# Kernel optimization log

Hardware: AMD Instinct MI355X
Metric: run time of the kernel (lower is better)

The kernel has to match this reference:

```python
import jax, jax.numpy as jnp
import numpy as np

N = 100000      # nodes
E = 1600000     # edges
F_IN = 64       # num_features
H = 64          # hidden_channels
NG = 64         # graphs in batch
ALPHA = 0.5


def _lin_init(key, fan_in, fan_out):
    kw, kb = jax.random.split(key)
    bound = 1.0 / np.sqrt(fan_in)
    w = jax.random.uniform(kw, (fan_in, fan_out), jnp.float32, -bound, bound)
    b = jax.random.uniform(kb, (fan_out,), jnp.float32, -bound, bound)
    return w, b


def setup_inputs() -> dict:
    key = jax.random.key(0)
    ks = jax.random.split(key, 12)
    x = jax.random.normal(ks[0], (N, F_IN), dtype=jnp.float32)
    edge_index = jax.random.randint(ks[1], (2, E), 0, N, dtype=jnp.int32)
    batch = jnp.sort(jax.random.randint(ks[2], (N,), 0, NG, dtype=jnp.int32))
    w1s, b1s = _lin_init(ks[3], F_IN, H)
    w1d, b1d = _lin_init(ks[4], F_IN, H)
    w2s, b2s = _lin_init(ks[5], H, H)
    w2d, b2d = _lin_init(ks[6], H, H)
    w3s, b3s = _lin_init(ks[7], H, H)
    w3d, b3d = _lin_init(ks[8], H, H)
    wl1, bl1 = _lin_init(ks[9], H, 5)
    wl2, bl2 = _lin_init(ks[10], 5, 1)
    return dict(x=x, edge_index=edge_index, batch=batch,
                w1s=w1s, b1s=b1s, w1d=w1d, b1d=b1d,
                w2s=w2s, b2s=b2s, w2d=w2d, b2d=b2d,
                w3s=w3s, b3s=b3s, w3d=w3d, b3d=b3d,
                wl1=wl1, bl1=bl1, wl2=wl2, bl2=bl2)


def _dir_gcn_conv(x, row, col, ws, bs, wd, bd):
    # directional norm: D_out^{-1/2} A D_in^{-1/2} (and same recipe for A^T)
    ones = jnp.ones((row.shape[0],), x.dtype)
    deg_out = jax.ops.segment_sum(ones, row, num_segments=N)  # row-sums of A
    deg_in = jax.ops.segment_sum(ones, col, num_segments=N)   # col-sums of A
    r_out = jnp.where(deg_out > 0, deg_out ** -0.5, 0.0)
    r_in = jnp.where(deg_in > 0, deg_in ** -0.5, 0.0)
    norm = r_out[row] * r_in[col]  # per-edge weight; identical for A and A^T norms
    msg = norm[:, None] * x[col]                       # [E, F]
    adj_x = jax.ops.segment_sum(msg, row, num_segments=N)
    msg_t = norm[:, None] * x[row]
    adj_t_x = jax.ops.segment_sum(msg_t, col, num_segments=N)
    return ALPHA * (adj_x @ ws + bs) + (1.0 - ALPHA) * (adj_t_x @ wd + bd)


def reference(x, edge_index, batch,
              w1s, b1s, w1d, b1d,
              w2s, b2s, w2d, b2d,
              w3s, b3s, w3d, b3d,
              wl1, bl1, wl2, bl2):
    row, col = edge_index[0], edge_index[1]
    h = jax.nn.relu(_dir_gcn_conv(x, row, col, w1s, b1s, w1d, b1d))
    h = jax.nn.relu(_dir_gcn_conv(h, row, col, w2s, b2s, w2d, b2d))
    h = jax.nn.relu(_dir_gcn_conv(h, row, col, w3s, b3s, w3d, b3d))
    g = jax.ops.segment_max(h, batch, num_segments=NG)  # global max pool [NG, H]
    g = jax.nn.relu(g @ wl1 + bl1)
    return g @ wl2 + bl2  # [NG, 1]
```

## Files before the change

### kernel.cpp

```cpp
#include <hip/hip_runtime.h>

#define N_NODES 100000
#define N_EDGES 1600000
#define EPAD    (N_EDGES + NB * BW)
#define HDIM    64
#define NGRAPH  64
#define BW      256
#define NB      391
#define NBLK    256
#define CHUNK   ((N_EDGES + NBLK - 1) / NBLK)
#define MTILES  (N_NODES / 16)

typedef _Float16 h16;
typedef _Float16 h16x4 __attribute__((ext_vector_type(4)));
typedef _Float16 h16x8 __attribute__((ext_vector_type(8)));
typedef float    f32x4 __attribute__((ext_vector_type(4)));

__global__ __launch_bounds__(512) void bucket_count(const int* __restrict__ ei,
                                                    int* __restrict__ cntTabA,
                                                    int* __restrict__ cntTabT) {
    __shared__ int cA[NB], cT[NB];
    const int tid = threadIdx.x;
    for (int i = tid; i < NB; i += 512) { cA[i] = 0; cT[i] = 0; }
    __syncthreads();
    const int e0 = blockIdx.x * CHUNK, e1 = min(e0 + CHUNK, N_EDGES);
    for (int e = e0 + tid; e < e1; e += 512) {
        int r = ei[e];
        int c = ei[N_EDGES + e];
        atomicAdd(&cA[r >> 8], 1);
        atomicAdd(&cT[c >> 8], 1);
    }
    __syncthreads();
    for (int b = tid; b < NB; b += 512) {
        cntTabA[b * NBLK + blockIdx.x] = cA[b];
        cntTabT[b * NBLK + blockIdx.x] = cT[b];
    }
}

__global__ __launch_bounds__(256) void chunk_scan(int* __restrict__ cntTabA,
                                                  int* __restrict__ cntTabT,
                                                  int* __restrict__ tot) {
    __shared__ int s[256];
    const int b = blockIdx.x, d = blockIdx.y, tid = threadIdx.x;
    int* tab = d ? cntTabT : cntTabA;
    int v = tab[b * NBLK + tid];
    s[tid] = v;
    __syncthreads();
    for (int off = 1; off < 256; off <<= 1) {
        int t = (tid >= off) ? s[tid - off] : 0;
        __syncthreads();
        s[tid] += t;
        __syncthreads();
    }
    tab[b * NBLK + tid] = s[tid] - v;
    if (tid == 255) tot[d * 512 + b] = s[255];
}

__global__ __launch_bounds__(512) void start_scan(const int* __restrict__ tot,
                                                  int* __restrict__ bktStartA,
                                                  int* __restrict__ bktStartT) {
    __shared__ int s[512];
    const int tid = threadIdx.x;
    int v = (tid < NB) ? tot[tid] : 0;
    s[tid] = v;
    __syncthreads();
    for (int off = 1; off < 512; off <<= 1) {
        int t = (tid >= off) ? s[tid - off] : 0;
        __syncthreads();
        s[tid] += t;
        __syncthreads();
    }
    if (tid < NB) bktStartA[tid] = s[tid] - v;
    if (tid == 0) bktStartA[NB] = N_EDGES;
    __syncthreads();
    int v2 = (tid < NB) ? tot[512 + tid] : 0;
    s[tid] = v2;
    __syncthreads();
    for (int off = 1; off < 512; off <<= 1) {
        int t = (tid >= off) ? s[tid - off] : 0;
        __syncthreads();
        s[tid] += t;
        __syncthreads();
    }
    if (tid < NB) bktStartT[tid] = s[tid] - v2;
    if (tid == 0) bktStartT[NB] = N_EDGES;
}

__global__ __launch_bounds__(512) void bucketize_write(const int* __restrict__ ei,
                                                       const int* __restrict__ cntTabA,
                                                       const int* __restrict__ cntTabT,
                                                       const int* __restrict__ bktStartA,
                                                       const int* __restrict__ bktStartT,
                                                       int2* __restrict__ bktA,
                                                       int2* __restrict__ bktT) {
    __shared__ int bA[NB], bT[NB];
    const int tid = threadIdx.x;
    for (int i = tid; i < NB; i += 512) {
        bA[i] = bktStartA[i] + cntTabA[i * NBLK + blockIdx.x];
        bT[i] = bktStartT[i] + cntTabT[i * NBLK + blockIdx.x];
    }
    __syncthreads();
    const int e0 = blockIdx.x * CHUNK, e1 = min(e0 + CHUNK, N_EDGES);
    for (int e = e0 + tid; e < e1; e += 512) {
        int r = ei[e];
        int c = ei[N_EDGES + e];
        int pA = atomicAdd(&bA[r >> 8], 1);
        bktA[pA] = make_int2(r, c);
        int pT = atomicAdd(&bT[c >> 8], 1);
        bktT[pT] = make_int2(c, r);
    }
}

__global__ __launch_bounds__(256) void bucket_deg_ptr(
        const int* __restrict__ bktStartA, const int* __restrict__ bktStartT,
        const int2* __restrict__ bktA, const int2* __restrict__ bktT,
        int* __restrict__ deg_out, int* __restrict__ deg_in,
        float* __restrict__ r_out, float* __restrict__ r_in,
        int* __restrict__ rowptrP, int* __restrict__ colptrP) {
    __shared__ int c[BW];
    __shared__ int s[256];
    const int b = blockIdx.x, d = blockIdx.y, tid = threadIdx.x;
    const int* bs = d ? bktStartT : bktStartA;
    const int2* bkt = d ? bktT : bktA;
    int* deg = d ? deg_in : deg_out;
    float* rr = d ? r_in : r_out;
    int* ptr = d ? colptrP : rowptrP;
    const int node0 = b * BW;
    c[tid] = 0;
    __syncthreads();
    const int i0 = bs[b], i1 = bs[b + 1];
    for (int i = i0 + tid; i < i1; i += 256) atomicAdd(&c[bkt[i].x - node0], 1);
    __syncthreads();
    int n = node0 + tid, dg = c[tid];
    int pad = dg + (dg & 1);
    if (n < N_NODES) {
        deg[n] = dg;
        rr[n] = dg > 0 ? rsqrtf((float)dg) : 0.0f;
    } else pad = 0;
    s[tid] = pad;
    __syncthreads();
    for (int off = 1; off < 256; off <<= 1) {
        int t = (tid >= off) ? s[tid - off] : 0;
        __syncthreads();
        s[tid] += t;
        __syncthreads();
    }
    if (n < N_NODES) ptr[n] = i0 + b * BW + (s[tid] - pad);
}

__global__ __launch_bounds__(512) void bucket_scatter(
        const int* __restrict__ rowptrP, const int* __restrict__ colptrP,
        const float* __restrict__ r_out, const float* __restrict__ r_in,
        const int* __restrict__ bktStartA, const int* __restrict__ bktStartT,
        const int2* __restrict__ bktA, const int2* __restrict__ bktT,
        int2* __restrict__ recA, int2* __restrict__ recT) {
    __shared__ int cur[BW];
    __shared__ float rwt[BW];
    const int b = blockIdx.x, d = blockIdx.y, tid = threadIdx.x;
    const int* ptr = d ? colptrP : rowptrP;
    const float* rt = d ? r_in : r_out;
    const float* rs = d ? r_out : r_in;
    const int* bs = d ? bktStartT : bktStartA;
    const int2* bkt = d ? bktT : bktA;
    int2* rec = d ? recT : recA;
    const int node0 = b * BW;
    if (tid < BW) {
        int n = node0 + tid;
        cur[tid] = (n < N_NODES) ? ptr[n] : 0;
        rwt[tid] = (n < N_NODES) ? rt[n] : 0.0f;
    }
    __syncthreads();
    const int i0 = bs[b], i1 = bs[b + 1];
    for (int i = i0 + tid; i < i1; i += 512) {
        int2 e = bkt[i];
        float w = rwt[e.x - node0] * rs[e.y];
        int p = atomicAdd(&cur[e.x - node0], 1);
        rec[p] = make_int2(e.y << 7, __float_as_int(w));
    }
}

__global__ __launch_bounds__(256) void cast_kernel(const float4* __restrict__ x,
                                                   h16x4* __restrict__ xh,
                                                   unsigned* __restrict__ g) {
    if (blockIdx.x == 0) {
        for (int j = threadIdx.x; j < NGRAPH * HDIM; j += 256) g[j] = 0u;
    }
    int i = blockIdx.x * 256 + threadIdx.x;
    if (i < N_NODES * 16) {
        float4 v = x[i];
        h16x4 o;
        o.x = (h16)v.x; o.y = (h16)v.y; o.z = (h16)v.z; o.w = (h16)v.w;
        xh[i] = o;
    }
}

__global__ __launch_bounds__(256) void wprep_kernel(
        const float* __restrict__ w1s, const float* __restrict__ w1d,
        const float* __restrict__ w2s, const float* __restrict__ w2d,
        const float* __restrict__ w3s, const float* __restrict__ w3d,
        const float* __restrict__ b1s, const float* __restrict__ b1d,
        const float* __restrict__ b2s, const float* __restrict__ b2d,
        const float* __restrict__ b3s, const float* __restrict__ b3d,
        h16* __restrict__ WT, float* __restrict__ bc) {
    const int l = blockIdx.y;
    const float* ws = l == 0 ? w1s : l == 1 ? w2s : w3s;
    const float* wd = l == 0 ? w1d : l == 1 ? w2d : w3d;
    int e = blockIdx.x * 256 + threadIdx.x;
    if (e < 8192) {
        int f = e >> 7, k = e & 127;
        float v = (k < 64) ? ws[k * 64 + f] : wd[(k - 64) * 64 + f];
        WT[l * 8192 + f * 128 + k] = (h16)(0.5f * v);
    }
    if (blockIdx.x == 0 && threadIdx.x < 64) {
        const float* bs = l == 0 ? b1s : l == 1 ? b2s : b3s;
        const float* bd = l == 0 ? b1d : l == 1 ? b2d : b3d;
        bc[l * 64 + threadIdx.x] = 0.5f * (bs[threadIdx.x] + bd[threadIdx.x]);
    }
}

__device__ __forceinline__ void fma4h(float4& a, float w, h16x4 f) {
    a.x = fmaf(w, (float)f.x, a.x);
    a.y = fmaf(w, (float)f.y, a.y);
    a.z = fmaf(w, (float)f.z, a.z);
    a.w = fmaf(w, (float)f.w, a.w);
}

__device__ __forceinline__ float4 red_s(float4 v) {
    v.x += __shfl_xor(v.x, 16); v.y += __shfl_xor(v.y, 16);
    v.z += __shfl_xor(v.z, 16); v.w += __shfl_xor(v.w, 16);
    v.x += __shfl_xor(v.x, 32); v.y += __shfl_xor(v.y, 32);
    v.z += __shfl_xor(v.z, 32); v.w += __shfl_xor(v.w, 32);
    return v;
}

__device__ __forceinline__ h16x4 ld_h4(const char* __restrict__ p) {
    return *(const h16x4*)p;
}

__device__ __forceinline__ float4 agg_dir(const char* __restrict__ hb,
                                          const int2* __restrict__ rec,
                                          int start, int deg, int q, int s, int sh) {
    float4 a0 = {0.f,0.f,0.f,0.f}, a1 = {0.f,0.f,0.f,0.f};
    float4 a2 = {0.f,0.f,0.f,0.f}, a3 = {0.f,0.f,0.f,0.f};
    const int4* rec4 = (const int4*)(rec + start);
    const int qb = q * 8;
    int k = 0;
    for (; k + 16 <= deg; k += 16) {
        int4 p0 = rec4[(k >> 1) + s];
        int4 p1 = rec4[(k >> 1) + 4 + s];
        h16x4 f0 = ld_h4(hb + (p0.x << sh) + qb);
        h16x4 f1 = ld_h4(hb + (p0.z << sh) + qb);
        h16x4 f2 = ld_h4(hb + (p1.x << sh) + qb);
        h16x4 f3 = ld_h4(hb + (p1.z << sh) + qb);
        fma4h(a0, __int_as_float(p0.y), f0);
        fma4h(a1, __int_as_float(p0.w), f1);
        fma4h(a2, __int_as_float(p1.y), f2);
        fma4h(a3, __int_as_float(p1.w), f3);
    }
    if (k + 8 <= deg) {
        int4 p = rec4[(k >> 1) + s];
        h16x4 f0 = ld_h4(hb + (p.x << sh) + qb);
        h16x4 f1 = ld_h4(hb + (p.z << sh) + qb);
        fma4h(a0, __int_as_float(p.y), f0);
        fma4h(a1, __int_as_float(p.w), f1);
        k += 8;
    }
    int r = deg - k;
    if (2 * s < r) {
        int4 p = rec4[(k >> 1) + s];
        h16x4 f0 = ld_h4(hb + (p.x << sh) + qb);
        fma4h(a2, __int_as_float(p.y), f0);
        if (2 * s + 1 < r) {
            h16x4 f1 = ld_h4(hb + (p.z << sh) + qb);
            fma4h(a3, __int_as_float(p.w), f1);
        }
    }
    a0.x += a1.x; a0.y += a1.y; a0.z += a1.z; a0.w += a1.w;
    a2.x += a3.x; a2.y += a3.y; a2.z += a3.z; a2.w += a3.w;
    a0.x += a2.x; a0.y += a2.y; a0.z += a2.z; a0.w += a2.w;
    return red_s(a0);
}

__global__ __launch_bounds__(256) void agg_kernel(
        const char* __restrict__ h_in, char* __restrict__ acc_out, int sh,
        const int* __restrict__ rowptrP, const int* __restrict__ deg_out,
        const int2* __restrict__ recA,
        const int* __restrict__ colptrP, const int* __restrict__ deg_in,
        const int2* __restrict__ recT) {
    const int tid  = threadIdx.x;
    const int wid  = (blockIdx.x << 2) + (tid >> 6);
    const int lane = tid & 63;
    const int node = wid >> 1;
    const int dir  = wid & 1;
    const int q = lane & 15;
    const int s = lane >> 4;

    const int* ptr = dir ? colptrP : rowptrP;
    const int* deg = dir ? deg_in : deg_out;
    const int2* rec = dir ? recT : recA;

    float4 a = agg_dir(h_in, rec, ptr[node], deg[node], q, s, sh);
    if (s == 0) {
        h16x4 pk;
        pk.x = (h16)a.x; pk.y = (h16)a.y; pk.z = (h16)a.z; pk.w = (h16)a.w;
        *(h16x4*)(acc_out + (size_t)node * 256 + dir * 128 + q * 8) = pk;
    }
}

__global__ __launch_bounds__(256) void gemm_kernel(char* __restrict__ acc,
                                                   const h16* __restrict__ WT,
                                                   const float* __restrict__ bc,
                                                   const int* __restrict__ batch,
                                                   unsigned* __restrict__ g,
                                                   int do_pool) {
    const int lane = threadIdx.x & 63;
    const int wid = (blockIdx.x * 256 + threadIdx.x) >> 6;
    const int nW = gridDim.x * 4;
    const int m = lane & 15, t = lane >> 4;

    h16x8 bfrag[4][4];
    float bb[4];
#pragma unroll
    for (int nt = 0; nt < 4; nt++) {
        bb[nt] = bc[nt * 16 + m];
#pragma unroll
        for (int kk = 0; kk < 4; kk++)
            bfrag[nt][kk] = *(const h16x8*)(WT + (nt * 16 + m) * 128 + kk * 32 + t * 8);
    }

    for (int tile = wid; tile < MTILES; tile += nW) {
        char* arow = acc + (size_t)tile * 16 * 256;
        const int node0 = tile * 16;
        int b0 = 0, b15 = 0;
        if (do_pool) { b0 = batch[node0]; b15 = batch[node0 + 15]; }
        h16x8 afrag[4];
#pragma unroll
        for (int kk = 0; kk < 4; kk++)
            afrag[kk] = *(const h16x8*)(arow + m * 256 + kk * 64 + t * 16);
#pragma unroll
        for (int nt = 0; nt < 4; nt++) {
            f32x4 c = {0.f, 0.f, 0.f, 0.f};
#pragma unroll
            for (int kk = 0; kk < 4; kk++)
                c = __builtin_amdgcn_mfma_f32_16x16x32_f16(afrag[kk], bfrag[nt][kk], c, 0, 0, 0);
            float ov[4];
#pragma unroll
            for (int r = 0; r < 4; r++) {
                ov[r] = fmaxf(c[r] + bb[nt], 0.0f);
                *(h16*)(arow + (t * 4 + r) * 256 + (nt * 16 + m) * 2) = (h16)ov[r];
            }
            if (do_pool) {
                if (b0 == b15) {
                    float mx = fmaxf(fmaxf(ov[0], ov[1]), fmaxf(ov[2], ov[3]));
                    mx = fmaxf(mx, __shfl_xor(mx, 16));
                    mx = fmaxf(mx, __shfl_xor(mx, 32));
                    if (t == 0)
                        atomicMax(&g[b0 * HDIM + nt * 16 + m], __float_as_uint(mx));
                } else {
#pragma unroll
                    for (int r = 0; r < 4; r++)
                        atomicMax(&g[batch[node0 + t * 4 + r] * HDIM + nt * 16 + m],
                                  __float_as_uint(ov[r]));
                }
            }
        }
    }
}

__global__ __launch_bounds__(64) void mlp_kernel(const unsigned* __restrict__ g,
                                                 const float* __restrict__ wl1,
                                                 const float* __restrict__ bl1,
                                                 const float* __restrict__ wl2,
                                                 const float* __restrict__ bl2,
                                                 float* __restrict__ out) {
    int t = threadIdx.x;
    float gv[HDIM];
#pragma unroll
    for (int k = 0; k < HDIM; k++) gv[k] = __uint_as_float(g[t * HDIM + k]);
    float o = bl2[0];
#pragma unroll
    for (int j = 0; j < 5; j++) {
        float hj = bl1[j];
#pragma unroll
        for (int k = 0; k < HDIM; k++) hj += gv[k] * wl1[k * 5 + j];
        hj = fmaxf(hj, 0.0f);
        o += hj * wl2[j];
    }
    out[t] = o;
}

extern "C" void kernel_launch(void* const* d_in, const int* in_sizes, int n_in,
                              void* d_out, int out_size, void* d_ws, size_t ws_size,
                              hipStream_t stream) {
    const float* x   = (const float*)d_in[0];
    const int*   ei  = (const int*)d_in[1];
    const int*   bat = (const int*)d_in[2];
    const float* w1s = (const float*)d_in[3];
    const float* b1s = (const float*)d_in[4];
    const float* w1d = (const float*)d_in[5];
    const float* b1d = (const float*)d_in[6];
    const float* w2s = (const float*)d_in[7];
    const float* b2s = (const float*)d_in[8];
    const float* w2d = (const float*)d_in[9];
    const float* b2d = (const float*)d_in[10];
    const float* w3s = (const float*)d_in[11];
    const float* b3s = (const float*)d_in[12];
    const float* w3d = (const float*)d_in[13];
    const float* b3d = (const float*)d_in[14];
    const float* wl1 = (const float*)d_in[15];
    const float* bl1 = (const float*)d_in[16];
    const float* wl2 = (const float*)d_in[17];
    const float* bl2 = (const float*)d_in[18];
    float* out = (float*)d_out;

    char* p = (char*)d_ws;
    int*   deg_out = (int*)p;              p += N_NODES * 4;
    int*   deg_in  = (int*)p;              p += N_NODES * 4;
    int*   rowptrP = (int*)p;              p += N_NODES * 4;
    int*   colptrP = (int*)p;              p += N_NODES * 4;
    float* r_out   = (float*)p;            p += N_NODES * 4;
    float* r_in    = (float*)p;            p += N_NODES * 4;
    int*   cntTabA = (int*)p;              p += (size_t)NB * NBLK * 4;
    int*   cntTabT = (int*)p;              p += (size_t)NB * NBLK * 4;
    int*   totTab  = (int*)p;              p += 1024 * 4;
    int*   bktStartA = (int*)p;            p += 512 * 4;
    int*   bktStartT = (int*)p;            p += 512 * 4;
    int2*  recA    = (int2*)p;             p += (size_t)EPAD * 8;
    int2*  recT    = (int2*)p;             p += (size_t)EPAD * 8;
    char*  bufP    = p;
    int2*  bktA    = (int2*)p;
    int2*  bktT    = (int2*)(p + (size_t)N_EDGES * 8);
    p += 2 * (size_t)N_EDGES * 8;
    char*  bufQ    = p;
    h16*   xh      = (h16*)p;
    p += 2 * (size_t)N_EDGES * 8;
    unsigned* g    = (unsigned*)p;         p += NGRAPH * HDIM * 4;
    h16*   WT      = (h16*)p;              p += 3 * 8192 * 2;
    float* bc      = (float*)p;            p += 3 * 64 * 4;

    cast_kernel<<<(N_NODES * 16 + 255) / 256, 256, 0, stream>>>(
        (const float4*)x, (h16x4*)xh, g);
    dim3 gw(32, 3);
    wprep_kernel<<<gw, 256, 0, stream>>>(w1s, w1d, w2s, w2d, w3s, w3d,
                                         b1s, b1d, b2s, b2d, b3s, b3d, WT, bc);

    bucket_count<<<NBLK, 512, 0, stream>>>(ei, cntTabA, cntTabT);
    dim3 gb2(NB, 2);
    chunk_scan<<<gb2, 256, 0, stream>>>(cntTabA, cntTabT, totTab);
    start_scan<<<1, 512, 0, stream>>>(totTab, bktStartA, bktStartT);
    bucketize_write<<<NBLK, 512, 0, stream>>>(ei, cntTabA, cntTabT,
                                              bktStartA, bktStartT, bktA, bktT);

    dim3 gb(NB, 2);
    bucket_deg_ptr<<<gb, 256, 0, stream>>>(bktStartA, bktStartT, bktA, bktT,
                                           deg_out, deg_in, r_out, r_in,
                                           rowptrP, colptrP);
    bucket_scatter<<<gb, 512, 0, stream>>>(
        rowptrP, colptrP, r_out, r_in, bktStartA, bktStartT, bktA, bktT, recA, recT);

    const int agrid = N_NODES * 2 / 4;
    agg_kernel<<<agrid, 256, 0, stream>>>((const char*)xh, bufP, 0,
                                          rowptrP, deg_out, recA, colptrP, deg_in, recT);
    gemm_kernel<<<256, 256, 0, stream>>>(bufP, WT, bc, bat, g, 0);
    agg_kernel<<<agrid, 256, 0, stream>>>(bufP, bufQ, 1,
                                          rowptrP, deg_out, recA, colptrP, deg_in, recT);
    gemm_kernel<<<256, 256, 0, stream>>>(bufQ, WT + 8192, bc + 64, bat, g, 0);
    agg_kernel<<<agrid, 256, 0, stream>>>(bufQ, bufP, 1,
                                          rowptrP, deg_out, recA, colptrP, deg_in, recT);
    gemm_kernel<<<256, 256, 0, stream>>>(bufP, WT + 16384, bc + 128, bat, g, 1);

    mlp_kernel<<<1, 64, 0, stream>>>(g, wl1, bl1, wl2, bl2, out);
}
```

Before: 489.8 us.

## Aggregate both edge directions per wavefront with 16-byte feature gathers

The aggregation kernel now gives each wavefront one node and handles both the forward (A) and transposed (A^T) directions, instead of one wavefront per node and direction. Each lane loads 8 fp16 features (16 bytes) instead of 4. That uses 8 lanes per row and 8 edge slots, so each iteration covers 16 edges per direction. The two directions' gathers are interleaved in a shared loop to raise memory-level parallelism, and the grid is halved. The cost is more registers per lane, a three-step shuffle reduction, and possible imbalance when in-degree and out-degree differ.

```diff
diff --git a/kernel.cpp b/kernel.cpp
--- a/kernel.cpp
+++ b/kernel.cpp
@@ -218,14 +218,20 @@
     }
 }
 
-__device__ __forceinline__ void fma4h(float4& a, float w, h16x4 f) {
-    a.x = fmaf(w, (float)f.x, a.x);
-    a.y = fmaf(w, (float)f.y, a.y);
-    a.z = fmaf(w, (float)f.z, a.z);
-    a.w = fmaf(w, (float)f.w, a.w);
-}
-
-__device__ __forceinline__ float4 red_s(float4 v) {
+__device__ __forceinline__ void fma8h(float4& a0, float4& a1, float w, h16x8 f) {
+    a0.x = fmaf(w, (float)f[0], a0.x);
+    a0.y = fmaf(w, (float)f[1], a0.y);
+    a0.z = fmaf(w, (float)f[2], a0.z);
+    a0.w = fmaf(w, (float)f[3], a0.w);
+    a1.x = fmaf(w, (float)f[4], a1.x);
+    a1.y = fmaf(w, (float)f[5], a1.y);
+    a1.z = fmaf(w, (float)f[6], a1.z);
+    a1.w = fmaf(w, (float)f[7], a1.w);
+}
+
+__device__ __forceinline__ float4 red3(float4 v) {
+    v.x += __shfl_xor(v.x, 8);  v.y += __shfl_xor(v.y, 8);
+    v.z += __shfl_xor(v.z, 8);  v.w += __shfl_xor(v.w, 8);
     v.x += __shfl_xor(v.x, 16); v.y += __shfl_xor(v.y, 16);
     v.z += __shfl_xor(v.z, 16); v.w += __shfl_xor(v.w, 16);
     v.x += __shfl_xor(v.x, 32); v.y += __shfl_xor(v.y, 32);
@@ -233,52 +239,31 @@
     return v;
 }
 
-__device__ __forceinline__ h16x4 ld_h4(const char* __restrict__ p) {
-    return *(const h16x4*)p;
-}
-
-__device__ __forceinline__ float4 agg_dir(const char* __restrict__ hb,
-                                          const int2* __restrict__ rec,
-                                          int start, int deg, int q, int s, int sh) {
-    float4 a0 = {0.f,0.f,0.f,0.f}, a1 = {0.f,0.f,0.f,0.f};
-    float4 a2 = {0.f,0.f,0.f,0.f}, a3 = {0.f,0.f,0.f,0.f};
-    const int4* rec4 = (const int4*)(rec + start);
-    const int qb = q * 8;
-    int k = 0;
-    for (; k + 16 <= deg; k += 16) {
-        int4 p0 = rec4[(k >> 1) + s];
-        int4 p1 = rec4[(k >> 1) + 4 + s];
-        h16x4 f0 = ld_h4(hb + (p0.x << sh) + qb);
-        h16x4 f1 = ld_h4(hb + (p0.z << sh) + qb);
-        h16x4 f2 = ld_h4(hb + (p1.x << sh) + qb);
-        h16x4 f3 = ld_h4(hb + (p1.z << sh) + qb);
-        fma4h(a0, __int_as_float(p0.y), f0);
-        fma4h(a1, __int_as_float(p0.w), f1);
-        fma4h(a2, __int_as_float(p1.y), f2);
-        fma4h(a3, __int_as_float(p1.w), f3);
-    }
-    if (k + 8 <= deg) {
-        int4 p = rec4[(k >> 1) + s];
-        h16x4 f0 = ld_h4(hb + (p.x << sh) + qb);
-        h16x4 f1 = ld_h4(hb + (p.z << sh) + qb);
-        fma4h(a0, __int_as_float(p.y), f0);
-        fma4h(a1, __int_as_float(p.w), f1);
-        k += 8;
-    }
+__device__ __forceinline__ void agg_step16(const char* __restrict__ hb,
+                                           const int4* __restrict__ r4, int k,
+                                           int s, int qb, int sh,
+                                           float4& a0, float4& a1) {
+    int4 p = r4[(k >> 1) + s];
+    h16x8 f0 = *(const h16x8*)(hb + (p.x << sh) + qb);
+    h16x8 f1 = *(const h16x8*)(hb + (p.z << sh) + qb);
+    fma8h(a0, a1, __int_as_float(p.y), f0);
+    fma8h(a0, a1, __int_as_float(p.w), f1);
+}
+
+__device__ __forceinline__ void agg_rem(const char* __restrict__ hb,
+                                        const int4* __restrict__ r4, int k,
+                                        int deg, int s, int qb, int sh,
+                                        float4& a0, float4& a1) {
     int r = deg - k;
     if (2 * s < r) {
-        int4 p = rec4[(k >> 1) + s];
-        h16x4 f0 = ld_h4(hb + (p.x << sh) + qb);
-        fma4h(a2, __int_as_float(p.y), f0);
+        int4 p = r4[(k >> 1) + s];
+        h16x8 f0 = *(const h16x8*)(hb + (p.x << sh) + qb);
+        fma8h(a0, a1, __int_as_float(p.y), f0);
         if (2 * s + 1 < r) {
-            h16x4 f1 = ld_h4(hb + (p.z << sh) + qb);
-            fma4h(a3, __int_as_float(p.w), f1);
+            h16x8 f1 = *(const h16x8*)(hb + (p.z << sh) + qb);
+            fma8h(a0, a1, __int_as_float(p.w), f1);
         }
     }
-    a0.x += a1.x; a0.y += a1.y; a0.z += a1.z; a0.w += a1.w;
-    a2.x += a3.x; a2.y += a3.y; a2.z += a3.z; a2.w += a3.w;
-    a0.x += a2.x; a0.y += a2.y; a0.z += a2.z; a0.w += a2.w;
-    return red_s(a0);
 }
 
 __global__ __launch_bounds__(256) void agg_kernel(
@@ -288,22 +273,48 @@
         const int* __restrict__ colptrP, const int* __restrict__ deg_in,
         const int2* __restrict__ recT) {
     const int tid  = threadIdx.x;
-    const int wid  = (blockIdx.x << 2) + (tid >> 6);
+    const int node = (blockIdx.x << 2) + (tid >> 6);
     const int lane = tid & 63;
-    const int node = wid >> 1;
-    const int dir  = wid & 1;
-    const int q = lane & 15;
-    const int s = lane >> 4;
-
-    const int* ptr = dir ? colptrP : rowptrP;
-    const int* deg = dir ? deg_in : deg_out;
-    const int2* rec = dir ? recT : recA;
-
-    float4 a = agg_dir(h_in, rec, ptr[node], deg[node], q, s, sh);
+    const int q = lane & 7;
+    const int s = lane >> 3;
+    const int qb = q * 16;
+
+    const int startA = rowptrP[node], dA = deg_out[node];
+    const int startT = colptrP[node], dT = deg_in[node];
+    const int4* rA4 = (const int4*)(recA + startA);
+    const int4* rT4 = (const int4*)(recT + startT);
+
+    float4 aA0 = {0.f,0.f,0.f,0.f}, aA1 = {0.f,0.f,0.f,0.f};
+    float4 aT0 = {0.f,0.f,0.f,0.f}, aT1 = {0.f,0.f,0.f,0.f};
+
+    int kA = 0, kT = 0;
+    for (; kA + 16 <= dA && kT + 16 <= dT; kA += 16, kT += 16) {
+        int4 pA = rA4[(kA >> 1) + s];
+        int4 pT = rT4[(kT >> 1) + s];
+        h16x8 fA0 = *(const h16x8*)(h_in + (pA.x << sh) + qb);
+        h16x8 fA1 = *(const h16x8*)(h_in + (pA.z << sh) + qb);
+        h16x8 fT0 = *(const h16x8*)(h_in + (pT.x << sh) + qb);
+        h16x8 fT1 = *(const h16x8*)(h_in + (pT.z << sh) + qb);
+        fma8h(aA0, aA1, __int_as_float(pA.y), fA0);
+        fma8h(aA0, aA1, __int_as_float(pA.w), fA1);
+        fma8h(aT0, aT1, __int_as_float(pT.y), fT0);
+        fma8h(aT0, aT1, __int_as_float(pT.w), fT1);
+    }
+    for (; kA + 16 <= dA; kA += 16) agg_step16(h_in, rA4, kA, s, qb, sh, aA0, aA1);
+    for (; kT + 16 <= dT; kT += 16) agg_step16(h_in, rT4, kT, s, qb, sh, aT0, aT1);
+    agg_rem(h_in, rA4, kA, dA, s, qb, sh, aA0, aA1);
+    agg_rem(h_in, rT4, kT, dT, s, qb, sh, aT0, aT1);
+
+    aA0 = red3(aA0); aA1 = red3(aA1);
+    aT0 = red3(aT0); aT1 = red3(aT1);
     if (s == 0) {
-        h16x4 pk;
-        pk.x = (h16)a.x; pk.y = (h16)a.y; pk.z = (h16)a.z; pk.w = (h16)a.w;
-        *(h16x4*)(acc_out + (size_t)node * 256 + dir * 128 + q * 8) = pk;
+        h16x8 pk;
+        pk[0] = (h16)aA0.x; pk[1] = (h16)aA0.y; pk[2] = (h16)aA0.z; pk[3] = (h16)aA0.w;
+        pk[4] = (h16)aA1.x; pk[5] = (h16)aA1.y; pk[6] = (h16)aA1.z; pk[7] = (h16)aA1.w;
+        *(h16x8*)(acc_out + (size_t)node * 256 + qb) = pk;
+        pk[0] = (h16)aT0.x; pk[1] = (h16)aT0.y; pk[2] = (h16)aT0.z; pk[3] = (h16)aT0.w;
+        pk[4] = (h16)aT1.x; pk[5] = (h16)aT1.y; pk[6] = (h16)aT1.z; pk[7] = (h16)aT1.w;
+        *(h16x8*)(acc_out + (size_t)node * 256 + 128 + qb) = pk;
     }
 }
 
@@ -458,7 +469,7 @@
     bucket_scatter<<<gb, 512, 0, stream>>>(
         rowptrP, colptrP, r_out, r_in, bktStartA, bktStartT, bktA, bktT, recA, recT);
 
-    const int agrid = N_NODES * 2 / 4;
+    const int agrid = N_NODES / 4;
     agg_kernel<<<agrid, 256, 0, stream>>>((const char*)xh, bufP, 0,
                                           rowptrP, deg_out, recA, colptrP, deg_in, recT);
     gemm_kernel<<<256, 256, 0, stream>>>(bufP, WT, bc, bat, g, 0);
```

Result: slower. 527.7 us (+7.7%).

## Make aggregation persistent with software-prefetched pointers and first edge records

Applied to the files above, without the earlier changes.

Replaces the one-wave-per-(node,direction) aggregation launch with a fixed grid of 8192 waves. Each wave processes a contiguous range of about 24 units. Within a wave, the pointer and degree for the unit two ahead and the first two edge-record vectors for the next unit are loaded before the current unit is computed. This hides the dependent index-load latency chain and cuts the cost of launching many short waves. In exchange it adds register pressure and gives less parallelism per unit, and load imbalance across waves can arise from degree variance.

```diff
diff --git a/kernel.cpp b/kernel.cpp
--- a/kernel.cpp
+++ b/kernel.cpp
@@ -10,6 +10,9 @@
 #define NBLK    256
 #define CHUNK   ((N_EDGES + NBLK - 1) / NBLK)
 #define MTILES  (N_NODES / 16)
+#define AGG_BLK 2048
+#define AGG_WAVES (AGG_BLK * 4)
+#define NUNITS  (N_NODES * 2)
 
 typedef _Float16 h16;
 typedef _Float16 h16x4 __attribute__((ext_vector_type(4)));
@@ -237,17 +240,13 @@
     return *(const h16x4*)p;
 }
 
-__device__ __forceinline__ float4 agg_dir(const char* __restrict__ hb,
-                                          const int2* __restrict__ rec,
-                                          int start, int deg, int q, int s, int sh) {
+__device__ __forceinline__ float4 agg_unit(const char* __restrict__ hb,
+                                           const int4* __restrict__ r4,
+                                           int deg, int4 p0, int4 p1,
+                                           int s, int qb, int sh) {
     float4 a0 = {0.f,0.f,0.f,0.f}, a1 = {0.f,0.f,0.f,0.f};
     float4 a2 = {0.f,0.f,0.f,0.f}, a3 = {0.f,0.f,0.f,0.f};
-    const int4* rec4 = (const int4*)(rec + start);
-    const int qb = q * 8;
-    int k = 0;
-    for (; k + 16 <= deg; k += 16) {
-        int4 p0 = rec4[(k >> 1) + s];
-        int4 p1 = rec4[(k >> 1) + 4 + s];
+    if (deg >= 16) {
         h16x4 f0 = ld_h4(hb + (p0.x << sh) + qb);
         h16x4 f1 = ld_h4(hb + (p0.z << sh) + qb);
         h16x4 f2 = ld_h4(hb + (p1.x << sh) + qb);
@@ -256,23 +255,47 @@
         fma4h(a1, __int_as_float(p0.w), f1);
         fma4h(a2, __int_as_float(p1.y), f2);
         fma4h(a3, __int_as_float(p1.w), f3);
-    }
-    if (k + 8 <= deg) {
-        int4 p = rec4[(k >> 1) + s];
-        h16x4 f0 = ld_h4(hb + (p.x << sh) + qb);
-        h16x4 f1 = ld_h4(hb + (p.z << sh) + qb);
-        fma4h(a0, __int_as_float(p.y), f0);
-        fma4h(a1, __int_as_float(p.w), f1);
-        k += 8;
-    }
-    int r = deg - k;
-    if (2 * s < r) {
-        int4 p = rec4[(k >> 1) + s];
-        h16x4 f0 = ld_h4(hb + (p.x << sh) + qb);
-        fma4h(a2, __int_as_float(p.y), f0);
-        if (2 * s + 1 < r) {
-            h16x4 f1 = ld_h4(hb + (p.z << sh) + qb);
-            fma4h(a3, __int_as_float(p.w), f1);
+        int k = 16;
+        for (; k + 16 <= deg; k += 16) {
+            int4 P0 = r4[(k >> 1) + s];
+            int4 P1 = r4[(k >> 1) + 4 + s];
+            h16x4 g0 = ld_h4(hb + (P0.x << sh) + qb);
+            h16x4 g1 = ld_h4(hb + (P0.z << sh) + qb);
+            h16x4 g2 = ld_h4(hb + (P1.x << sh) + qb);
+            h16x4 g3 = ld_h4(hb + (P1.z << sh) + qb);
+            fma4h(a0, __int_as_float(P0.y), g0);
+            fma4h(a1, __int_as_float(P0.w), g1);
+            fma4h(a2, __int_as_float(P1.y), g2);
+            fma4h(a3, __int_as_float(P1.w), g3);
+        }
+        if (k + 8 <= deg) {
+            int4 P = r4[(k >> 1) + s];
+            fma4h(a0, __int_as_float(P.y), ld_h4(hb + (P.x << sh) + qb));
+            fma4h(a1, __int_as_float(P.w), ld_h4(hb + (P.z << sh) + qb));
+            k += 8;
+        }
+        int r = deg - k;
+        if (2 * s < r) {
+            int4 P = r4[(k >> 1) + s];
+            fma4h(a2, __int_as_float(P.y), ld_h4(hb + (P.x << sh) + qb));
+            if (2 * s + 1 < r)
+                fma4h(a3, __int_as_float(P.w), ld_h4(hb + (P.z << sh) + qb));
+        }
+    } else if (deg >= 8) {
+        fma4h(a0, __int_as_float(p0.y), ld_h4(hb + (p0.x << sh) + qb));
+        fma4h(a1, __int_as_float(p0.w), ld_h4(hb + (p0.z << sh) + qb));
+        int r = deg - 8;
+        if (2 * s < r) {
+            fma4h(a2, __int_as_float(p1.y), ld_h4(hb + (p1.x << sh) + qb));
+            if (2 * s + 1 < r)
+                fma4h(a3, __int_as_float(p1.w), ld_h4(hb + (p1.z << sh) + qb));
+        }
+    } else {
+        int r = deg;
+        if (2 * s < r) {
+            fma4h(a2, __int_as_float(p0.y), ld_h4(hb + (p0.x << sh) + qb));
+            if (2 * s + 1 < r)
+                fma4h(a3, __int_as_float(p0.w), ld_h4(hb + (p0.z << sh) + qb));
         }
     }
     a0.x += a1.x; a0.y += a1.y; a0.z += a1.z; a0.w += a1.w;
@@ -290,20 +313,41 @@
     const int tid  = threadIdx.x;
     const int wid  = (blockIdx.x << 2) + (tid >> 6);
     const int lane = tid & 63;
-    const int node = wid >> 1;
-    const int dir  = wid & 1;
-    const int q = lane & 15;
     const int s = lane >> 4;
-
-    const int* ptr = dir ? colptrP : rowptrP;
-    const int* deg = dir ? deg_in : deg_out;
-    const int2* rec = dir ? recT : recA;
-
-    float4 a = agg_dir(h_in, rec, ptr[node], deg[node], q, s, sh);
-    if (s == 0) {
-        h16x4 pk;
-        pk.x = (h16)a.x; pk.y = (h16)a.y; pk.z = (h16)a.z; pk.w = (h16)a.w;
-        *(h16x4*)(acc_out + (size_t)node * 256 + dir * 128 + q * 8) = pk;
+    const int qb = (lane & 15) * 8;
+
+    const int u0 = (int)(((long long)wid * NUNITS) / AGG_WAVES);
+    const int u1 = (int)(((long long)(wid + 1) * NUNITS) / AGG_WAVES);
+
+    int dirC = (u0 >= N_NODES);
+    int nC   = u0 - (dirC ? N_NODES : 0);
+    int stC  = (dirC ? colptrP : rowptrP)[nC];
+    int dgC  = (dirC ? deg_in : deg_out)[nC];
+    int un = u0 + 1; if (un >= NUNITS) un = NUNITS - 1;
+    int dirN = (un >= N_NODES);
+    int nN   = un - (dirN ? N_NODES : 0);
+    int stN  = (dirN ? colptrP : rowptrP)[nN];
+    int dgN  = (dirN ? deg_in : deg_out)[nN];
+    const int4* rc = (const int4*)((dirC ? recT : recA) + stC);
+    int4 p0 = rc[s], p1 = rc[4 + s];
+
+    for (int u = u0; u < u1; ++u) {
+        int uu = u + 2; if (uu >= NUNITS) uu = NUNITS - 1;
+        int dir2 = (uu >= N_NODES);
+        int n2   = uu - (dir2 ? N_NODES : 0);
+        int st2  = (dir2 ? colptrP : rowptrP)[n2];
+        int dg2  = (dir2 ? deg_in : deg_out)[n2];
+        const int4* rn = (const int4*)((dirN ? recT : recA) + stN);
+        int4 q0 = rn[s], q1 = rn[4 + s];
+
+        float4 a = agg_unit(h_in, rc, dgC, p0, p1, s, qb, sh);
+        if (s == 0) {
+            h16x4 pk;
+            pk.x = (h16)a.x; pk.y = (h16)a.y; pk.z = (h16)a.z; pk.w = (h16)a.w;
+            *(h16x4*)(acc_out + (size_t)nC * 256 + dirC * 128 + qb) = pk;
+        }
+        dirC = dirN; nC = nN; dgC = dgN; rc = rn; p0 = q0; p1 = q1;
+        dirN = dir2; nN = n2; stN = st2; dgN = dg2;
     }
 }
 
@@ -458,15 +502,14 @@
     bucket_scatter<<<gb, 512, 0, stream>>>(
         rowptrP, colptrP, r_out, r_in, bktStartA, bktStartT, bktA, bktT, recA, recT);
 
-    const int agrid = N_NODES * 2 / 4;
-    agg_kernel<<<agrid, 256, 0, stream>>>((const char*)xh, bufP, 0,
-                                          rowptrP, deg_out, recA, colptrP, deg_in, recT);
+    agg_kernel<<<AGG_BLK, 256, 0, stream>>>((const char*)xh, bufP, 0,
+                                            rowptrP, deg_out, recA, colptrP, deg_in, recT);
     gemm_kernel<<<256, 256, 0, stream>>>(bufP, WT, bc, bat, g, 0);
-    agg_kernel<<<agrid, 256, 0, stream>>>(bufP, bufQ, 1,
-                                          rowptrP, deg_out, recA, colptrP, deg_in, recT);
+    agg_kernel<<<AGG_BLK, 256, 0, stream>>>(bufP, bufQ, 1,
+                                            rowptrP, deg_out, recA, colptrP, deg_in, recT);
     gemm_kernel<<<256, 256, 0, stream>>>(bufQ, WT + 8192, bc + 64, bat, g, 0);
-    agg_kernel<<<agrid, 256, 0, stream>>>(bufQ, bufP, 1,
-                                          rowptrP, deg_out, recA, colptrP, deg_in, recT);
+    agg_kernel<<<AGG_BLK, 256, 0, stream>>>(bufQ, bufP, 1,
+                                            rowptrP, deg_out, recA, colptrP, deg_in, recT);
     gemm_kernel<<<256, 256, 0, stream>>>(bufP, WT + 16384, bc + 128, bat, g, 1);
 
     mlp_kernel<<<1, 64, 0, stream>>>(g, wl1, bl1, wl2, bl2, out);
```

Measured after the change: 494.7 us. No clear change (+1.0%).

## Replace two-pass bucket sort CSR build with global-atomic counting sort

Applied to the files above, without the earlier changes.

Graph preprocessing no longer bucketizes edges into 256-node bins in LDS. It now counts degrees with global atomics, scans per-node padded degrees, and scatters edge records directly using per-node global atomic cursors. This drops the intermediate bucket arrays and one full pass over the edges, but adds contention on global atomics and random global writes. Edge order within a row becomes nondeterministic, as it already was before.

```diff
diff --git a/kernel.cpp b/kernel.cpp
--- a/kernel.cpp
+++ b/kernel.cpp
@@ -2,49 +2,58 @@
 
 #define N_NODES 100000
 #define N_EDGES 1600000
-#define EPAD    (N_EDGES + NB * BW)
+#define NB      391
+#define EPAD    (N_EDGES + NB * 256)
 #define HDIM    64
 #define NGRAPH  64
-#define BW      256
-#define NB      391
-#define NBLK    256
-#define CHUNK   ((N_EDGES + NBLK - 1) / NBLK)
 #define MTILES  (N_NODES / 16)
+#define EBLK    3125
 
 typedef _Float16 h16;
 typedef _Float16 h16x4 __attribute__((ext_vector_type(4)));
 typedef _Float16 h16x8 __attribute__((ext_vector_type(8)));
 typedef float    f32x4 __attribute__((ext_vector_type(4)));
 
-__global__ __launch_bounds__(512) void bucket_count(const int* __restrict__ ei,
-                                                    int* __restrict__ cntTabA,
-                                                    int* __restrict__ cntTabT) {
-    __shared__ int cA[NB], cT[NB];
-    const int tid = threadIdx.x;
-    for (int i = tid; i < NB; i += 512) { cA[i] = 0; cT[i] = 0; }
-    __syncthreads();
-    const int e0 = blockIdx.x * CHUNK, e1 = min(e0 + CHUNK, N_EDGES);
-    for (int e = e0 + tid; e < e1; e += 512) {
-        int r = ei[e];
-        int c = ei[N_EDGES + e];
-        atomicAdd(&cA[r >> 8], 1);
-        atomicAdd(&cT[c >> 8], 1);
-    }
-    __syncthreads();
-    for (int b = tid; b < NB; b += 512) {
-        cntTabA[b * NBLK + blockIdx.x] = cA[b];
-        cntTabT[b * NBLK + blockIdx.x] = cT[b];
-    }
-}
-
-__global__ __launch_bounds__(256) void chunk_scan(int* __restrict__ cntTabA,
-                                                  int* __restrict__ cntTabT,
-                                                  int* __restrict__ tot) {
+__global__ __launch_bounds__(256) void cast_kernel(const float4* __restrict__ x,
+                                                   h16x4* __restrict__ xh,
+                                                   unsigned* __restrict__ g,
+                                                   int* __restrict__ degz) {
+    if (blockIdx.x == 0) {
+        for (int j = threadIdx.x; j < NGRAPH * HDIM; j += 256) g[j] = 0u;
+    }
+    int i = blockIdx.x * 256 + threadIdx.x;
+    if (i < 2 * N_NODES) degz[i] = 0;
+    if (i < N_NODES * 16) {
+        float4 v = x[i];
+        h16x4 o;
+        o.x = (h16)v.x; o.y = (h16)v.y; o.z = (h16)v.z; o.w = (h16)v.w;
+        xh[i] = o;
+    }
+}
+
+__global__ __launch_bounds__(512) void deg_count(const int* __restrict__ ei,
+                                                 int* __restrict__ deg_out,
+                                                 int* __restrict__ deg_in) {
+    int e = blockIdx.x * 512 + threadIdx.x;
+    atomicAdd(&deg_out[ei[e]], 1);
+    atomicAdd(&deg_in[ei[N_EDGES + e]], 1);
+}
+
+__global__ __launch_bounds__(256) void node_scan(
+        const int* __restrict__ deg_out, const int* __restrict__ deg_in,
+        float* __restrict__ r_out, float* __restrict__ r_in,
+        int* __restrict__ rowptrP, int* __restrict__ colptrP,
+        int* __restrict__ totP) {
     __shared__ int s[256];
     const int b = blockIdx.x, d = blockIdx.y, tid = threadIdx.x;
-    int* tab = d ? cntTabT : cntTabA;
-    int v = tab[b * NBLK + tid];
-    s[tid] = v;
+    const int* deg = d ? deg_in : deg_out;
+    float* rr = d ? r_in : r_out;
+    int* ptr = d ? colptrP : rowptrP;
+    const int n = b * 256 + tid;
+    int dg = (n < N_NODES) ? deg[n] : 0;
+    if (n < N_NODES) rr[n] = dg > 0 ? rsqrtf((float)dg) : 0.0f;
+    int pad = dg + (dg & 1);
+    s[tid] = pad;
     __syncthreads();
     for (int off = 1; off < 256; off <<= 1) {
         int t = (tid >= off) ? s[tid - off] : 0;
@@ -52,13 +61,13 @@
         s[tid] += t;
         __syncthreads();
     }
-    tab[b * NBLK + tid] = s[tid] - v;
-    if (tid == 255) tot[d * 512 + b] = s[255];
+    if (n < N_NODES) ptr[n] = s[tid] - pad;
+    if (tid == 255) totP[d * 512 + b] = s[255];
 }
 
 __global__ __launch_bounds__(512) void start_scan(const int* __restrict__ tot,
-                                                  int* __restrict__ bktStartA,
-                                                  int* __restrict__ bktStartT) {
+                                                  int* __restrict__ basePA,
+                                                  int* __restrict__ basePT) {
     __shared__ int s[512];
     const int tid = threadIdx.x;
     int v = (tid < NB) ? tot[tid] : 0;
@@ -70,8 +79,7 @@
         s[tid] += t;
         __syncthreads();
     }
-    if (tid < NB) bktStartA[tid] = s[tid] - v;
-    if (tid == 0) bktStartA[NB] = N_EDGES;
+    if (tid < NB) basePA[tid] = s[tid] - v;
     __syncthreads();
     int v2 = (tid < NB) ? tot[512 + tid] : 0;
     s[tid] = v2;
@@ -82,116 +90,35 @@
         s[tid] += t;
         __syncthreads();
     }
-    if (tid < NB) bktStartT[tid] = s[tid] - v2;
-    if (tid == 0) bktStartT[NB] = N_EDGES;
-}
-
-__global__ __launch_bounds__(512) void bucketize_write(const int* __restrict__ ei,
-                                                       const int* __restrict__ cntTabA,
-                                                       const int* __restrict__ cntTabT,
-                                                       const int* __restrict__ bktStartA,
-                                                       const int* __restrict__ bktStartT,
-                                                       int2* __restrict__ bktA,
-                                                       int2* __restrict__ bktT) {
-    __shared__ int bA[NB], bT[NB];
-    const int tid = threadIdx.x;
-    for (int i = tid; i < NB; i += 512) {
-        bA[i] = bktStartA[i] + cntTabA[i * NBLK + blockIdx.x];
-        bT[i] = bktStartT[i] + cntTabT[i * NBLK + blockIdx.x];
-    }
-    __syncthreads();
-    const int e0 = blockIdx.x * CHUNK, e1 = min(e0 + CHUNK, N_EDGES);
-    for (int e = e0 + tid; e < e1; e += 512) {
-        int r = ei[e];
-        int c = ei[N_EDGES + e];
-        int pA = atomicAdd(&bA[r >> 8], 1);
-        bktA[pA] = make_int2(r, c);
-        int pT = atomicAdd(&bT[c >> 8], 1);
-        bktT[pT] = make_int2(c, r);
-    }
-}
-
-__global__ __launch_bounds__(256) void bucket_deg_ptr(
-        const int* __restrict__ bktStartA, const int* __restrict__ bktStartT,
-        const int2* __restrict__ bktA, const int2* __restrict__ bktT,
-        int* __restrict__ deg_out, int* __restrict__ deg_in,
-        float* __restrict__ r_out, float* __restrict__ r_in,
-        int* __restrict__ rowptrP, int* __restrict__ colptrP) {
-    __shared__ int c[BW];
-    __shared__ int s[256];
-    const int b = blockIdx.x, d = blockIdx.y, tid = threadIdx.x;
-    const int* bs = d ? bktStartT : bktStartA;
-    const int2* bkt = d ? bktT : bktA;
-    int* deg = d ? deg_in : deg_out;
-    float* rr = d ? r_in : r_out;
-    int* ptr = d ? colptrP : rowptrP;
-    const int node0 = b * BW;
-    c[tid] = 0;
-    __syncthreads();
-    const int i0 = bs[b], i1 = bs[b + 1];
-    for (int i = i0 + tid; i < i1; i += 256) atomicAdd(&c[bkt[i].x - node0], 1);
-    __syncthreads();
-    int n = node0 + tid, dg = c[tid];
-    int pad = dg + (dg & 1);
-    if (n < N_NODES) {
-        deg[n] = dg;
-        rr[n] = dg > 0 ? rsqrtf((float)dg) : 0.0f;
-    } else pad = 0;
-    s[tid] = pad;
-    __syncthreads();
-    for (int off = 1; off < 256; off <<= 1) {
-        int t = (tid >= off) ? s[tid - off] : 0;
-        __syncthreads();
-        s[tid] += t;
-        __syncthreads();
-    }
-    if (n < N_NODES) ptr[n] = i0 + b * BW + (s[tid] - pad);
-}
-
-__global__ __launch_bounds__(512) void bucket_scatter(
-        const int* __restrict__ rowptrP, const int* __restrict__ colptrP,
-        const float* __restrict__ r_out, const float* __restrict__ r_in,
-        const int* __restrict__ bktStartA, const int* __restrict__ bktStartT,
-        const int2* __restrict__ bktA, const int2* __restrict__ bktT,
-        int2* __restrict__ recA, int2* __restrict__ recT) {
-    __shared__ int cur[BW];
-    __shared__ float rwt[BW];
-    const int b = blockIdx.x, d = blockIdx.y, tid = threadIdx.x;
-    const int* ptr = d ? colptrP : rowptrP;
-    const float* rt = d ? r_in : r_out;
-    const float* rs = d ? r_out : r_in;
-    const int* bs = d ? bktStartT : bktStartA;
-    const int2* bkt = d ? bktT : bktA;
-    int2* rec = d ? recT : recA;
-    const int node0 = b * BW;
-    if (tid < BW) {
-        int n = node0 + tid;
-        cur[tid] = (n < N_NODES) ? ptr[n] : 0;
-        rwt[tid] = (n < N_NODES) ? rt[n] : 0.0f;
-    }
-    __syncthreads();
-    const int i0 = bs[b], i1 = bs[b + 1];
-    for (int i = i0 + tid; i < i1; i += 512) {
-        int2 e = bkt[i];
-        float w = rwt[e.x - node0] * rs[e.y];
-        int p = atomicAdd(&cur[e.x - node0], 1);
-        rec[p] = make_int2(e.y << 7, __float_as_int(w));
-    }
-}
-
-__global__ __launch_bounds__(256) void cast_kernel(const float4* __restrict__ x,
-                                                   h16x4* __restrict__ xh,
-                                                   unsigned* __restrict__ g) {
-    if (blockIdx.x == 0) {
-        for (int j = threadIdx.x; j < NGRAPH * HDIM; j += 256) g[j] = 0u;
-    }
-    int i = blockIdx.x * 256 + threadIdx.x;
-    if (i < N_NODES * 16) {
-        float4 v = x[i];
-        h16x4 o;
-        o.x = (h16)v.x; o.y = (h16)v.y; o.z = (h16)v.z; o.w = (h16)v.w;
-        xh[i] = o;
-    }
+    if (tid < NB) basePT[tid] = s[tid] - v2;
+}
+
+__global__ __launch_bounds__(256) void node_base(
+        const int* __restrict__ basePA, const int* __restrict__ basePT,
+        int* __restrict__ rowptrP, int* __restrict__ colptrP,
+        int* __restrict__ curA, int* __restrict__ curT) {
+    const int b = blockIdx.x, d = blockIdx.y;
+    const int n = b * 256 + threadIdx.x;
+    if (n >= N_NODES) return;
+    if (d == 0) { int v = rowptrP[n] + basePA[b]; rowptrP[n] = v; curA[n] = v; }
+    else        { int v = colptrP[n] + basePT[b]; colptrP[n] = v; curT[n] = v; }
+}
+
+__global__ __launch_bounds__(512) void edge_scatter(const int* __restrict__ ei,
+                                                    const float* __restrict__ r_out,
+                                                    const float* __restrict__ r_in,
+                                                    int* __restrict__ curA,
+                                                    int* __restrict__ curT,
+                                                    int2* __restrict__ recA,
+                                                    int2* __restrict__ recT) {
+    int e = blockIdx.x * 512 + threadIdx.x;
+    int r = ei[e];
+    int c = ei[N_EDGES + e];
+    float w = r_out[r] * r_in[c];
+    int pA = atomicAdd(&curA[r], 1);
+    recA[pA] = make_int2(c << 7, __float_as_int(w));
+    int pT = atomicAdd(&curT[c], 1);
+    recT[pT] = make_int2(r << 7, __float_as_int(w));
 }
 
 __global__ __launch_bounds__(256) void wprep_kernel(
@@ -420,16 +347,14 @@
     int*   colptrP = (int*)p;              p += N_NODES * 4;
     float* r_out   = (float*)p;            p += N_NODES * 4;
     float* r_in    = (float*)p;            p += N_NODES * 4;
-    int*   cntTabA = (int*)p;              p += (size_t)NB * NBLK * 4;
-    int*   cntTabT = (int*)p;              p += (size_t)NB * NBLK * 4;
-    int*   totTab  = (int*)p;              p += 1024 * 4;
-    int*   bktStartA = (int*)p;            p += 512 * 4;
-    int*   bktStartT = (int*)p;            p += 512 * 4;
+    int*   curA    = (int*)p;              p += (size_t)N_NODES * 4;
+    int*   curT    = (int*)p;              p += (size_t)N_NODES * 4;
+    int*   totP    = (int*)p;              p += 1024 * 4;
+    int*   basePA  = (int*)p;              p += 512 * 4;
+    int*   basePT  = (int*)p;              p += 512 * 4;
     int2*  recA    = (int2*)p;             p += (size_t)EPAD * 8;
     int2*  recT    = (int2*)p;             p += (size_t)EPAD * 8;
     char*  bufP    = p;
-    int2*  bktA    = (int2*)p;
-    int2*  bktT    = (int2*)(p + (size_t)N_EDGES * 8);
     p += 2 * (size_t)N_EDGES * 8;
     char*  bufQ    = p;
     h16*   xh      = (h16*)p;
@@ -439,24 +364,18 @@
     float* bc      = (float*)p;            p += 3 * 64 * 4;
 
     cast_kernel<<<(N_NODES * 16 + 255) / 256, 256, 0, stream>>>(
-        (const float4*)x, (h16x4*)xh, g);
+        (const float4*)x, (h16x4*)xh, g, deg_out);
     dim3 gw(32, 3);
     wprep_kernel<<<gw, 256, 0, stream>>>(w1s, w1d, w2s, w2d, w3s, w3d,
                                          b1s, b1d, b2s, b2d, b3s, b3d, WT, bc);
 
-    bucket_count<<<NBLK, 512, 0, stream>>>(ei, cntTabA, cntTabT);
-    dim3 gb2(NB, 2);
-    chunk_scan<<<gb2, 256, 0, stream>>>(cntTabA, cntTabT, totTab);
-    start_scan<<<1, 512, 0, stream>>>(totTab, bktStartA, bktStartT);
-    bucketize_write<<<NBLK, 512, 0, stream>>>(ei, cntTabA, cntTabT,
-                                              bktStartA, bktStartT, bktA, bktT);
-
+    deg_count<<<EBLK, 512, 0, stream>>>(ei, deg_out, deg_in);
     dim3 gb(NB, 2);
-    bucket_deg_ptr<<<gb, 256, 0, stream>>>(bktStartA, bktStartT, bktA, bktT,
-                                           deg_out, deg_in, r_out, r_in,
-                                           rowptrP, colptrP);
-    bucket_scatter<<<gb, 512, 0, stream>>>(
-        rowptrP, colptrP, r_out, r_in, bktStartA, bktStartT, bktA, bktT, recA, recT);
+    node_scan<<<gb, 256, 0, stream>>>(deg_out, deg_in, r_out, r_in,
+                                      rowptrP, colptrP, totP);
+    start_scan<<<1, 512, 0, stream>>>(totP, basePA, basePT);
+    node_base<<<gb, 256, 0, stream>>>(basePA, basePT, rowptrP, colptrP, curA, curT);
+    edge_scatter<<<EBLK, 512, 0, stream>>>(ei, r_out, r_in, curA, curT, recA, recT);
 
     const int agrid = N_NODES * 2 / 4;
     agg_kernel<<<agrid, 256, 0, stream>>>((const char*)xh, bufP, 0,
```

After: 739.7 us. +51.0%, slower.
